# Kernel optimization log

Hardware: AMD Instinct MI355X
Metric: run time of the kernel (lower is better)

Reference implementation:

```python
import jax, jax.numpy as jnp
import numpy as np

DIM = 1024
N_HEADS = 16
HEAD_DIM = DIM // N_HEADS


def setup_inputs() -> dict:
    key = jax.random.key(0)
    ks = jax.random.split(key, 7)
    B, S = 2, 2048
    scale = 0.02
    return {
        "q": jax.random.normal(ks[0], (B, S, DIM), dtype=jnp.float32),
        "k": jax.random.normal(ks[1], (B, S, DIM), dtype=jnp.float32),
        "v": jax.random.normal(ks[2], (B, S, DIM), dtype=jnp.float32),
        # torch nn.Linear weights are [out_features, in_features]; y = x @ W.T
        "wq": jax.random.normal(ks[3], (DIM, DIM), dtype=jnp.float32) * scale,
        "wk": jax.random.normal(ks[4], (DIM, DIM), dtype=jnp.float32) * scale,
        "wv": jax.random.normal(ks[5], (DIM, DIM), dtype=jnp.float32) * scale,
        "wo": jax.random.normal(ks[6], (DIM, DIM), dtype=jnp.float32) * scale,
    }


def reference(q, k, v, wq, wk, wv, wo):
    B, S, _ = q.shape
    H, D = N_HEADS, HEAD_DIM
    # projections (torch Linear: x @ W.T), reshape to [B, H, S, D]
    xq = (q @ wq.T).reshape(B, S, H, D).transpose(0, 2, 1, 3)
    xk = (k @ wk.T).reshape(B, S, H, D).transpose(0, 2, 1, 3)
    xv = (v @ wv.T).reshape(B, S, H, D).transpose(0, 2, 1, 3)
    # scaled dot-product attention with causal mask
    scores = jnp.einsum("bhqd,bhkd->bhqk", xq, xk) / jnp.sqrt(jnp.float32(D))
    causal = jnp.tril(jnp.ones((S, S), dtype=bool))
    scores = jnp.where(causal, scores, -jnp.inf)
    attn = jax.nn.softmax(scores.astype(jnp.float32), axis=-1).astype(xq.dtype)
    # dropout prob = 0.0 (eval-mode / deterministic reference)
    out = jnp.einsum("bhqk,bhkd->bhqd", attn, xv)
    out = out.transpose(0, 2, 1, 3).reshape(B, S, H * D)
    return out @ wo.T
```

## Files before the change

### kernel.cpp

```cpp
#include <hip/hip_runtime.h>
#include <hip/hip_bf16.h>
#include <stdint.h>


typedef short s16x8 __attribute__((ext_vector_type(8)));
typedef float f32x4 __attribute__((ext_vector_type(4)));

#define MFMA_BF16 __builtin_amdgcn_mfma_f32_16x16x32_bf16

static __device__ __forceinline__ unsigned short f2bf(float f) {
    union { float f; unsigned u; } x{f};
    unsigned r = x.u + 0x7fff + ((x.u >> 16) & 1);
    return (unsigned short)(r >> 16);
}
static __device__ __forceinline__ unsigned pk2h(float a, float b) {
    __hip_bfloat162 h = __float22bfloat162_rn(float2{a, b});
    return *(unsigned*)&h;
}

static __device__ __forceinline__ void ald16(unsigned short* lds, const unsigned short* g) {
    __builtin_amdgcn_global_load_lds(
        (const __attribute__((address_space(1))) unsigned int*)g,
        (__attribute__((address_space(3))) unsigned int*)lds, 16, 0, 0);
}

#define QSCL 0.18033688f

__global__ __launch_bounds__(256) void convert_all_kernel(
        const float* __restrict__ q, const float* __restrict__ k,
        const float* __restrict__ v,
        const float* __restrict__ wq, const float* __restrict__ wk,
        const float* __restrict__ wv, const float* __restrict__ wo,
        unsigned short* __restrict__ dst) {
    const size_t idx = ((size_t)blockIdx.x * 256 + threadIdx.x) * 8;
    const int region = (int)(idx >> 22);
    const float* src;
    size_t off;
    if (region == 0)      { src = q; off = idx; }
    else if (region == 1) { src = k; off = idx & 4194303; }
    else if (region == 2) { src = v; off = idx & 4194303; }
    else {
        const int wsel = (int)((idx >> 20) & 3);
        src = wsel == 0 ? wq : wsel == 1 ? wk : wsel == 2 ? wv : wo;
        off = idx & 1048575;
    }
    const float4* p = (const float4*)(src + off);
    float4 a = p[0], b = p[1];
    uint4 u;
    u.x = pk2h(a.x, a.y); u.y = pk2h(a.z, a.w);
    u.z = pk2h(b.x, b.y); u.w = pk2h(b.z, b.w);
    *(uint4*)(dst + idx) = u;
}

__global__ __launch_bounds__(256) void wconvert_kernel(
        const float* __restrict__ wq, const float* __restrict__ wk,
        const float* __restrict__ wv, const float* __restrict__ wo,
        unsigned short* __restrict__ Wb) {
    const size_t idx = ((size_t)blockIdx.x * 256 + threadIdx.x) * 8;
    const int region = (int)(idx >> 20);
    const size_t off = idx & 1048575;
    const float* src = region == 0 ? wq : region == 1 ? wk : region == 2 ? wv : wo;
    const float4* p = (const float4*)(src + off);
    float4 a = p[0], b = p[1];
    uint4 u;
    u.x = pk2h(a.x, a.y); u.y = pk2h(a.z, a.w);
    u.z = pk2h(b.x, b.y); u.w = pk2h(b.z, b.w);
    *(uint4*)(Wb + idx) = u;
}

__global__ __launch_bounds__(256) void proj3b_kernel(
        const unsigned short* __restrict__ Qb, const unsigned short* __restrict__ Kb,
        const unsigned short* __restrict__ Vb, const unsigned short* __restrict__ Wb,
        unsigned short* __restrict__ Xq, unsigned short* __restrict__ Xk,
        unsigned short* __restrict__ Xvt) {
    constexpr int Kd = 1024;
    __shared__ union {
        struct { unsigned short A[128 * 32]; unsigned short B[128 * 32]; } s;
        unsigned short T[4 * 64 * 68];
    } sm;

    const int z = blockIdx.z;
    const unsigned short* A  = z == 0 ? Qb : z == 1 ? Kb : Vb;
    const unsigned short* Bw = Wb + (size_t)z * 1048576;

    const int t = threadIdx.x;
    const int m0 = blockIdx.x * 128, n0 = blockIdx.y * 128;
    const int w = t >> 6, lane = t & 63, fr = lane & 15, g = lane >> 4;
    const int wm = (w >> 1) * 64, wn = (w & 1) * 64;
    const int brow = t >> 2;
    const int cB = (t & 3) ^ ((t >> 3) & 3);
    const int sB = g ^ ((fr >> 1) & 3);

    f32x4 acc[4][4] = {};

    for (int k0 = 0; k0 < Kd; k0 += 32) {
        ald16(sm.s.A + (size_t)w * 512,        A  + (size_t)(m0 + brow) * Kd + k0 + cB * 8);
        ald16(sm.s.A + 2048 + (size_t)w * 512, A  + (size_t)(m0 + 64 + brow) * Kd + k0 + cB * 8);
        ald16(sm.s.B + (size_t)w * 512,        Bw + (size_t)(n0 + brow) * Kd + k0 + cB * 8);
        ald16(sm.s.B + 2048 + (size_t)w * 512, Bw + (size_t)(n0 + 64 + brow) * Kd + k0 + cB * 8);
        __syncthreads();

        s16x8 af[4], bfv[4];
#pragma unroll
        for (int mi = 0; mi < 4; ++mi)
            af[mi] = *(const s16x8*)(sm.s.A + (wm + mi * 16 + fr) * 32 + sB * 8);
#pragma unroll
        for (int ni = 0; ni < 4; ++ni)
            bfv[ni] = *(const s16x8*)(sm.s.B + (wn + ni * 16 + fr) * 32 + sB * 8);
#pragma unroll
        for (int mi = 0; mi < 4; ++mi)
#pragma unroll
            for (int ni = 0; ni < 4; ++ni)
                acc[mi][ni] = MFMA_BF16(af[mi], bfv[ni], acc[mi][ni], 0, 0, 0);
        __syncthreads();
    }

    if (z != 2) {
        unsigned short* C = z ? Xk : Xq;
        const float osc = z == 0 ? QSCL : 1.0f;
#pragma unroll
        for (int mi = 0; mi < 4; ++mi)
#pragma unroll
            for (int ni = 0; ni < 4; ++ni)
#pragma unroll
                for (int reg = 0; reg < 4; ++reg)
                    C[(size_t)(m0 + wm + mi * 16 + g * 4 + reg) * 1024 +
                      n0 + wn + ni * 16 + fr] = f2bf(acc[mi][ni][reg] * osc);
    } else {
        unsigned short* T = sm.T + w * (64 * 68);
#pragma unroll
        for (int mi = 0; mi < 4; ++mi)
#pragma unroll
            for (int ni = 0; ni < 4; ++ni) {
                uint2 u;
                u.x = pk2h(acc[mi][ni][0], acc[mi][ni][1]);
                u.y = pk2h(acc[mi][ni][2], acc[mi][ni][3]);
                *(uint2*)(T + (ni * 16 + fr) * 68 + mi * 16 + g * 4) = u;
            }
        __asm__ __volatile__("" ::: "memory");
#pragma unroll
        for (int pass = 0; pass < 8; ++pass) {
            const int row = pass * 8 + (lane >> 3);
            const int chk = lane & 7;
            uint4 d = *(const uint4*)(T + row * 68 + chk * 8);
            *(uint4*)(Xvt + (size_t)(n0 + wn + row) * 4096 + m0 + wm + chk * 8) = d;
        }
    }
}

__global__ __launch_bounds__(256) void proj3_kernel(
        const float* __restrict__ q, const float* __restrict__ k, const float* __restrict__ v,
        const unsigned short* __restrict__ Wb,
        unsigned short* __restrict__ Xq, unsigned short* __restrict__ Xk,
        unsigned short* __restrict__ Xvt) {
    constexpr int Kd = 1024;
    __shared__ unsigned short lsA[128 * 40];
    __shared__ unsigned short lsB[128 * 32];
    __shared__ unsigned short Tls[4 * 64 * 68];

    const int z = blockIdx.z;
    const float* A = z == 0 ? q : z == 1 ? k : v;
    const unsigned short* Bw = Wb + (size_t)z * 1048576;

    const int t = threadIdx.x;
    const int m0 = blockIdx.x * 128, n0 = blockIdx.y * 128;
    const int w = t >> 6, lane = t & 63, fr = lane & 15, g = lane >> 4, fq = g * 8;
    const int wm = (w >> 1) * 64, wn = (w & 1) * 64;
    const int ar = t >> 1, ac = (t & 1) * 16;
    const int brow = t >> 2;
    const int cB = (t & 3) ^ ((t >> 3) & 3);
    const int sB = g ^ ((fr >> 1) & 3);

    f32x4 acc[4][4] = {};

    for (int k0 = 0; k0 < Kd; k0 += 32) {
        ald16(lsB + (size_t)w * 512,        Bw + (size_t)(n0 + brow) * Kd + k0 + cB * 8);
        ald16(lsB + 2048 + (size_t)w * 512, Bw + (size_t)(n0 + 64 + brow) * Kd + k0 + cB * 8);
        {
            const float4* pa = (const float4*)(A + (size_t)(m0 + ar) * Kd + k0 + ac);
            float4 a0 = pa[0], a1 = pa[1], a2 = pa[2], a3 = pa[3];
            uint4 u0, u1;
            u0.x = pk2h(a0.x, a0.y); u0.y = pk2h(a0.z, a0.w);
            u0.z = pk2h(a1.x, a1.y); u0.w = pk2h(a1.z, a1.w);
            u1.x = pk2h(a2.x, a2.y); u1.y = pk2h(a2.z, a2.w);
            u1.z = pk2h(a3.x, a3.y); u1.w = pk2h(a3.z, a3.w);
            *(uint4*)(lsA + ar * 40 + ac)     = u0;
            *(uint4*)(lsA + ar * 40 + ac + 8) = u1;
        }
        __syncthreads();

        s16x8 af[4], bfv[4];
#pragma unroll
        for (int mi = 0; mi < 4; ++mi)
            af[mi] = *(const s16x8*)(lsA + (wm + mi * 16 + fr) * 40 + fq);
#pragma unroll
        for (int ni = 0; ni < 4; ++ni)
            bfv[ni] = *(const s16x8*)(lsB + (wn + ni * 16 + fr) * 32 + sB * 8);
#pragma unroll
        for (int mi = 0; mi < 4; ++mi)
#pragma unroll
            for (int ni = 0; ni < 4; ++ni)
                acc[mi][ni] = MFMA_BF16(af[mi], bfv[ni], acc[mi][ni], 0, 0, 0);
        __syncthreads();
    }

    if (z != 2) {
        unsigned short* C = z ? Xk : Xq;
        const float osc = z == 0 ? QSCL : 1.0f;
#pragma unroll
        for (int mi = 0; mi < 4; ++mi)
#pragma unroll
            for (int ni = 0; ni < 4; ++ni)
#pragma unroll
                for (int reg = 0; reg < 4; ++reg)
                    C[(size_t)(m0 + wm + mi * 16 + g * 4 + reg) * 1024 +
                      n0 + wn + ni * 16 + fr] = f2bf(acc[mi][ni][reg] * osc);
    } else {
        unsigned short* T = Tls + w * (64 * 68);
#pragma unroll
        for (int mi = 0; mi < 4; ++mi)
#pragma unroll
            for (int ni = 0; ni < 4; ++ni) {
                uint2 u;
                u.x = pk2h(acc[mi][ni][0], acc[mi][ni][1]);
                u.y = pk2h(acc[mi][ni][2], acc[mi][ni][3]);
                *(uint2*)(T + (ni * 16 + fr) * 68 + mi * 16 + g * 4) = u;
            }
        __asm__ __volatile__("" ::: "memory");
#pragma unroll
        for (int pass = 0; pass < 8; ++pass) {
            const int row = pass * 8 + (lane >> 3);
            const int chk = lane & 7;
            uint4 d = *(const uint4*)(T + row * 68 + chk * 8);
            *(uint4*)(Xvt + (size_t)(n0 + wn + row) * 4096 + m0 + wm + chk * 8) = d;
        }
    }
}

static __device__ __forceinline__ void slab_tail(
        const f32x4 sf[4], int kt, int qt, int qrow, float& l_part,
        f32x4* oacc, unsigned short* Pw, const s16x8 vf[4][2], int fr, int g) {
    float e[4][4];
    const bool diag = (kt == qt);
#pragma unroll
    for (int m16 = 0; m16 < 4; ++m16)
#pragma unroll
        for (int r = 0; r < 4; ++r) {
            float x = sf[m16][r];
            if (diag) {
                const int keyg = kt * 64 + m16 * 16 + g * 4 + r;
                x = (keyg <= qrow) ? x : -1e30f;
            }
            const float ee = exp2f(x);
            e[m16][r] = ee;
            l_part += ee;
        }
#pragma unroll
    for (int m16 = 0; m16 < 4; ++m16) {
        uint2 u;
        u.x = pk2h(e[m16][0], e[m16][1]);
        u.y = pk2h(e[m16][2], e[m16][3]);
        const int ch = 2 * m16 + (g >> 1);
        *(uint2*)(Pw + fr * 64 + ((ch ^ (fr & 7)) * 8) + (g & 1) * 4) = u;
    }
    __asm__ __volatile__("" ::: "memory");
    s16x8 pf0 = *(const s16x8*)(Pw + fr * 64 + ((g ^ (fr & 7)) * 8));
    s16x8 pf1 = *(const s16x8*)(Pw + fr * 64 + (((4 + g) ^ (fr & 7)) * 8));
#pragma unroll
    for (int m16 = 0; m16 < 4; ++m16) {
        oacc[m16] = MFMA_BF16(vf[m16][0], pf0, oacc[m16], 0, 0, 0);
        oacc[m16] = MFMA_BF16(vf[m16][1], pf1, oacc[m16], 0, 0, 0);
    }
    __asm__ __volatile__("" ::: "memory");
}

__global__ __launch_bounds__(256, 2) void flash_attn_kernel(
        const unsigned short* __restrict__ Xq, const unsigned short* __restrict__ Xk,
        const unsigned short* __restrict__ Xvt, unsigned short* __restrict__ Oa) {
    __shared__ unsigned short Kls[64 * 64];
    __shared__ unsigned short Vls[64 * 64];
    __shared__ unsigned short Pls[4][16 * 64];

    const int t = threadIdx.x;
    const int bh = blockIdx.x;
    const int j = blockIdx.y;
    const int b = bh >> 4, h = bh & 15;
    const size_t rbase = (size_t)b * 2048;
    const int cbase = h * 64;

    const int w = t >> 6, lane = t & 63, fr = lane & 15, g = lane >> 4, fq = g * 8;
    const int qtH = 31 - j, qtL = j;
    const int qrowH = qtH * 64 + w * 16 + fr;
    const int qrowL = qtL * 64 + w * 16 + fr;

    const unsigned short* qpH = Xq + (rbase + qrowH) * 1024 + cbase;
    s16x8 qfH0 = *(const s16x8*)(qpH + fq);
    s16x8 qfH1 = *(const s16x8*)(qpH + 32 + fq);
    const unsigned short* qpL = Xq + (rbase + qrowL) * 1024 + cbase;
    s16x8 qfL0 = *(const s16x8*)(qpL + fq);
    s16x8 qfL1 = *(const s16x8*)(qpL + 32 + fq);

    float lH = 0.f, lL = 0.f;
    f32x4 oH[4] = {}, oL[4] = {};

    const int r0 = w * 16 + (lane >> 3), r1 = r0 + 8;
    const int s8 = lane & 7;
    const int c0 = s8 ^ (r0 & 7), c1 = s8 ^ (r1 & 7);
    const unsigned short* kbase = Xk + rbase * 1024 + cbase;
    const size_t vrow0 = (size_t)(cbase + r0) * 4096 + rbase + c0 * 8;
    const size_t vrow1 = (size_t)(cbase + r1) * 4096 + rbase + c1 * 8;

    uint4 kA, kB, vA, vB;
    kA = *(const uint4*)(kbase + (size_t)r0 * 1024 + c0 * 8);
    kB = *(const uint4*)(kbase + (size_t)r1 * 1024 + c1 * 8);
    vA = *(const uint4*)(Xvt + vrow0);
    vB = *(const uint4*)(Xvt + vrow1);

    for (int kt = 0; kt <= qtH; ++kt) {
        *(uint4*)(Kls + (w * 16) * 64 + lane * 8)     = kA;
        *(uint4*)(Kls + (w * 16 + 8) * 64 + lane * 8) = kB;
        *(uint4*)(Vls + (w * 16) * 64 + lane * 8)     = vA;
        *(uint4*)(Vls + (w * 16 + 8) * 64 + lane * 8) = vB;
        __syncthreads();

        if (kt < qtH) {
            const unsigned short* ks = kbase + (size_t)(kt + 1) * 65536;
            kA = *(const uint4*)(ks + (size_t)r0 * 1024 + c0 * 8);
            kB = *(const uint4*)(ks + (size_t)r1 * 1024 + c1 * 8);
            vA = *(const uint4*)(Xvt + vrow0 + (size_t)(kt + 1) * 64);
            vB = *(const uint4*)(Xvt + vrow1 + (size_t)(kt + 1) * 64);
        }

        const bool doL = (kt <= qtL);

        s16x8 kf[4][2], vf[4][2];
#pragma unroll
        for (int m16 = 0; m16 < 4; ++m16) {
            const int rr = m16 * 16 + fr;
            kf[m16][0] = *(const s16x8*)(Kls + rr * 64 + ((g ^ (fr & 7)) * 8));
            kf[m16][1] = *(const s16x8*)(Kls + rr * 64 + (((4 + g) ^ (fr & 7)) * 8));
            vf[m16][0] = *(const s16x8*)(Vls + rr * 64 + ((g ^ (fr & 7)) * 8));
            vf[m16][1] = *(const s16x8*)(Vls + rr * 64 + (((4 + g) ^ (fr & 7)) * 8));
        }

        f32x4 sH[4], sL[4];
#pragma unroll
        for (int m16 = 0; m16 < 4; ++m16) {
            f32x4 zz = {};
            zz = MFMA_BF16(kf[m16][0], qfH0, zz, 0, 0, 0);
            sH[m16] = MFMA_BF16(kf[m16][1], qfH1, zz, 0, 0, 0);
        }
        if (doL) {
#pragma unroll
            for (int m16 = 0; m16 < 4; ++m16) {
                f32x4 zz = {};
                zz = MFMA_BF16(kf[m16][0], qfL0, zz, 0, 0, 0);
                sL[m16] = MFMA_BF16(kf[m16][1], qfL1, zz, 0, 0, 0);
            }
        }
        slab_tail(sH, kt, qtH, qrowH, lH, oH, &Pls[w][0], vf, fr, g);
        if (doL)
            slab_tail(sL, kt, qtL, qrowL, lL, oL, &Pls[w][0], vf, fr, g);
        __syncthreads();
    }

    lH += __shfl_xor(lH, 16, 64);
    lH += __shfl_xor(lH, 32, 64);
    lL += __shfl_xor(lL, 16, 64);
    lL += __shfl_xor(lL, 32, 64);
    const float invH = 1.0f / lH, invL = 1.0f / lL;
#pragma unroll
    for (int m16 = 0; m16 < 4; ++m16) {
        uint2 u;
        u.x = pk2h(oH[m16][0] * invH, oH[m16][1] * invH);
        u.y = pk2h(oH[m16][2] * invH, oH[m16][3] * invH);
        *(uint2*)(Oa + (rbase + qrowH) * 1024 + cbase + m16 * 16 + g * 4) = u;
        uint2 u2;
        u2.x = pk2h(oL[m16][0] * invL, oL[m16][1] * invL);
        u2.y = pk2h(oL[m16][2] * invL, oL[m16][3] * invL);
        *(uint2*)(Oa + (rbase + qrowL) * 1024 + cbase + m16 * 16 + g * 4) = u2;
    }
}

__global__ __launch_bounds__(256) void outproj_kernel(
        const unsigned short* __restrict__ Oa, const unsigned short* __restrict__ Wo,
        float* __restrict__ out) {
    constexpr int Kd = 1024;
    __shared__ unsigned short lsA[64 * 32];
    __shared__ unsigned short lsB[128 * 32];

    const int t = threadIdx.x;
    const int m0 = blockIdx.x * 64, n0 = blockIdx.y * 128;
    const int w = t >> 6, lane = t & 63, fr = lane & 15, g = lane >> 4;
    const int wm = (w >> 1) * 32, wn = (w & 1) * 64;
    const int brow = t >> 2;
    const int cB = (t & 3) ^ ((t >> 3) & 3);
    const int sB = g ^ ((fr >> 1) & 3);

    f32x4 acc[2][4] = {};

    for (int k0 = 0; k0 < Kd; k0 += 32) {
        ald16(lsA + (size_t)w * 512,        Oa + (size_t)(m0 + brow) * Kd + k0 + cB * 8);
        ald16(lsB + (size_t)w * 512,        Wo + (size_t)(n0 + brow) * Kd + k0 + cB * 8);
        ald16(lsB + 2048 + (size_t)w * 512, Wo + (size_t)(n0 + 64 + brow) * Kd + k0 + cB * 8);
        __syncthreads();

        s16x8 af[2], bfv[4];
#pragma unroll
        for (int mi = 0; mi < 2; ++mi)
            af[mi] = *(const s16x8*)(lsA + (wm + mi * 16 + fr) * 32 + sB * 8);
#pragma unroll
        for (int ni = 0; ni < 4; ++ni)
            bfv[ni] = *(const s16x8*)(lsB + (wn + ni * 16 + fr) * 32 + sB * 8);
#pragma unroll
        for (int mi = 0; mi < 2; ++mi)
#pragma unroll
            for (int ni = 0; ni < 4; ++ni)
                acc[mi][ni] = MFMA_BF16(af[mi], bfv[ni], acc[mi][ni], 0, 0, 0);
        __syncthreads();
    }

#pragma unroll
    for (int mi = 0; mi < 2; ++mi)
#pragma unroll
        for (int ni = 0; ni < 4; ++ni)
#pragma unroll
            for (int reg = 0; reg < 4; ++reg)
                out[(size_t)(m0 + wm + mi * 16 + g * 4 + reg) * 1024 +
                    n0 + wn + ni * 16 + fr] = acc[mi][ni][reg];
}

extern "C" void kernel_launch(void* const* d_in, const int* in_sizes, int n_in,
                              void* d_out, int out_size, void* d_ws, size_t ws_size,
                              hipStream_t stream) {
    const float* q  = (const float*)d_in[0];
    const float* k  = (const float*)d_in[1];
    const float* v  = (const float*)d_in[2];
    const float* wq = (const float*)d_in[3];
    const float* wk = (const float*)d_in[4];
    const float* wv = (const float*)d_in[5];
    const float* wo = (const float*)d_in[6];
    float* out = (float*)d_out;

    if (ws_size >= (size_t)64 * 1024 * 1024) {
        unsigned short* base = (unsigned short*)d_ws;
        unsigned short* Qb  = base;
        unsigned short* Kb  = base + 4194304;
        unsigned short* Vb  = base + 8388608;
        unsigned short* Wb  = base + 12582912;
        unsigned short* Xq  = base + 16777216;
        unsigned short* Xk  = base + 20971520;
        unsigned short* Xvt = base + 25165824;
        unsigned short* Oa  = base + 29360128;

        convert_all_kernel<<<8192, 256, 0, stream>>>(q, k, v, wq, wk, wv, wo, base);
        proj3b_kernel<<<dim3(32, 8, 3), 256, 0, stream>>>(Qb, Kb, Vb, Wb, Xq, Xk, Xvt);
        flash_attn_kernel<<<dim3(32, 16), 256, 0, stream>>>(Xq, Xk, Xvt, Oa);
        outproj_kernel<<<dim3(64, 8), 256, 0, stream>>>(Oa, Wb + 3145728, out);
    } else {
        unsigned short* Wb  = (unsigned short*)d_ws;
        unsigned short* Xq  = Wb  + 4194304;
        unsigned short* Xk  = Xq  + 4194304;
        unsigned short* Xvt = Xk  + 4194304;
        unsigned short* Oa  = Xvt + 4194304;

        wconvert_kernel<<<2048, 256, 0, stream>>>(wq, wk, wv, wo, Wb);
        proj3_kernel<<<dim3(32, 8, 3), 256, 0, stream>>>(q, k, v, Wb, Xq, Xk, Xvt);
        flash_attn_kernel<<<dim3(32, 16), 256, 0, stream>>>(Xq, Xk, Xvt, Oa);
        outproj_kernel<<<dim3(64, 8), 256, 0, stream>>>(Oa, Wb + 3145728, out);
    }
}
```

Measured before the change: 213.6 us.

## Fuse convert, projection, attention and out-projection into one persistent kernel with grid barriers

Replaces the four kernel launches with a single persistent kernel of 512 blocks. The blocks pass through the phases (fp32-to-bf16 conversion, QKV projection using 64x128 tiles, flash attention, output projection) separated by atomic-counter grid barriers in workspace, which is zeroed by a memset before each launch. This removes launch gaps and inter-kernel tail effects. In exchange it relies on all 512 blocks being co-resident (two per CU), uses smaller projection tiles, has a spin barrier with a timeout guard, and drops the small-workspace fallback path.

```diff
diff --git a/kernel.cpp b/kernel.cpp
--- a/kernel.cpp
+++ b/kernel.cpp
@@ -17,7 +17,6 @@
     __hip_bfloat162 h = __float22bfloat162_rn(float2{a, b});
     return *(unsigned*)&h;
 }
-
 static __device__ __forceinline__ void ald16(unsigned short* lds, const unsigned short* g) {
     __builtin_amdgcn_global_load_lds(
         (const __attribute__((address_space(1))) unsigned int*)g,
@@ -25,90 +24,63 @@
 }
 
 #define QSCL 0.18033688f
-
-__global__ __launch_bounds__(256) void convert_all_kernel(
-        const float* __restrict__ q, const float* __restrict__ k,
-        const float* __restrict__ v,
-        const float* __restrict__ wq, const float* __restrict__ wk,
-        const float* __restrict__ wv, const float* __restrict__ wo,
-        unsigned short* __restrict__ dst) {
-    const size_t idx = ((size_t)blockIdx.x * 256 + threadIdx.x) * 8;
-    const int region = (int)(idx >> 22);
-    const float* src;
-    size_t off;
-    if (region == 0)      { src = q; off = idx; }
-    else if (region == 1) { src = k; off = idx & 4194303; }
-    else if (region == 2) { src = v; off = idx & 4194303; }
-    else {
-        const int wsel = (int)((idx >> 20) & 3);
-        src = wsel == 0 ? wq : wsel == 1 ? wk : wsel == 2 ? wv : wo;
-        off = idx & 1048575;
-    }
-    const float4* p = (const float4*)(src + off);
-    float4 a = p[0], b = p[1];
-    uint4 u;
-    u.x = pk2h(a.x, a.y); u.y = pk2h(a.z, a.w);
-    u.z = pk2h(b.x, b.y); u.w = pk2h(b.z, b.w);
-    *(uint4*)(dst + idx) = u;
-}
-
-__global__ __launch_bounds__(256) void wconvert_kernel(
-        const float* __restrict__ wq, const float* __restrict__ wk,
-        const float* __restrict__ wv, const float* __restrict__ wo,
-        unsigned short* __restrict__ Wb) {
-    const size_t idx = ((size_t)blockIdx.x * 256 + threadIdx.x) * 8;
-    const int region = (int)(idx >> 20);
-    const size_t off = idx & 1048575;
-    const float* src = region == 0 ? wq : region == 1 ? wk : region == 2 ? wv : wo;
-    const float4* p = (const float4*)(src + off);
-    float4 a = p[0], b = p[1];
-    uint4 u;
-    u.x = pk2h(a.x, a.y); u.y = pk2h(a.z, a.w);
-    u.z = pk2h(b.x, b.y); u.w = pk2h(b.z, b.w);
-    *(uint4*)(Wb + idx) = u;
-}
-
-__global__ __launch_bounds__(256) void proj3b_kernel(
-        const unsigned short* __restrict__ Qb, const unsigned short* __restrict__ Kb,
-        const unsigned short* __restrict__ Vb, const unsigned short* __restrict__ Wb,
-        unsigned short* __restrict__ Xq, unsigned short* __restrict__ Xk,
-        unsigned short* __restrict__ Xvt) {
+#define NBLK 512u
+
+union SM {
+    struct { unsigned short A[64 * 32]; unsigned short B[128 * 32]; } g;
+    unsigned short T[4 * 64 * 36];
+    struct { unsigned short K[64 * 64]; unsigned short V[64 * 64];
+             unsigned short P[4][16 * 64]; } f;
+};
+
+static __device__ __forceinline__ void grid_sync(unsigned* bar) {
+    __syncthreads();
+    if (threadIdx.x == 0) {
+        __threadfence();
+        __hip_atomic_fetch_add(bar, 1u, __ATOMIC_ACQ_REL, __HIP_MEMORY_SCOPE_AGENT);
+        int guard = 0;
+        while (__hip_atomic_load(bar, __ATOMIC_ACQUIRE, __HIP_MEMORY_SCOPE_AGENT) < NBLK) {
+            __builtin_amdgcn_s_sleep(8);
+            if (++guard > (1 << 22)) break;
+        }
+        __threadfence();
+    }
+    __syncthreads();
+}
+
+static __device__ void proj_tile64(int tile, SM& sm,
+        const unsigned short* __restrict__ ws, unsigned short* __restrict__ Xq,
+        unsigned short* __restrict__ Xk, unsigned short* __restrict__ Xvt) {
     constexpr int Kd = 1024;
-    __shared__ union {
-        struct { unsigned short A[128 * 32]; unsigned short B[128 * 32]; } s;
-        unsigned short T[4 * 64 * 68];
-    } sm;
-
-    const int z = blockIdx.z;
-    const unsigned short* A  = z == 0 ? Qb : z == 1 ? Kb : Vb;
-    const unsigned short* Bw = Wb + (size_t)z * 1048576;
+    const int z = tile >> 9;
+    const int m0 = (tile & 63) * 64, n0 = ((tile >> 6) & 7) * 128;
+    const unsigned short* A  = ws + (size_t)z * 4194304;
+    const unsigned short* Bw = ws + 12582912 + (size_t)z * 1048576;
 
     const int t = threadIdx.x;
-    const int m0 = blockIdx.x * 128, n0 = blockIdx.y * 128;
     const int w = t >> 6, lane = t & 63, fr = lane & 15, g = lane >> 4;
-    const int wm = (w >> 1) * 64, wn = (w & 1) * 64;
+    const int wm = (w >> 1) * 32, wn = (w & 1) * 64;
     const int brow = t >> 2;
     const int cB = (t & 3) ^ ((t >> 3) & 3);
     const int sB = g ^ ((fr >> 1) & 3);
 
-    f32x4 acc[4][4] = {};
+    f32x4 acc[2][4] = {};
 
     for (int k0 = 0; k0 < Kd; k0 += 32) {
-        ald16(sm.s.A + (size_t)w * 512,        A  + (size_t)(m0 + brow) * Kd + k0 + cB * 8);
-        ald16(sm.s.A + 2048 + (size_t)w * 512, A  + (size_t)(m0 + 64 + brow) * Kd + k0 + cB * 8);
-        ald16(sm.s.B + (size_t)w * 512,        Bw + (size_t)(n0 + brow) * Kd + k0 + cB * 8);
-        ald16(sm.s.B + 2048 + (size_t)w * 512, Bw + (size_t)(n0 + 64 + brow) * Kd + k0 + cB * 8);
-        __syncthreads();
-
-        s16x8 af[4], bfv[4];
-#pragma unroll
-        for (int mi = 0; mi < 4; ++mi)
-            af[mi] = *(const s16x8*)(sm.s.A + (wm + mi * 16 + fr) * 32 + sB * 8);
+        ald16(sm.g.A + (size_t)w * 512,        A  + (size_t)(m0 + brow) * Kd + k0 + cB * 8);
+        ald16(sm.g.B + (size_t)w * 512,        Bw + (size_t)(n0 + brow) * Kd + k0 + cB * 8);
+        ald16(sm.g.B + 2048 + (size_t)w * 512, Bw + (size_t)(n0 + 64 + brow) * Kd + k0 + cB * 8);
+        __syncthreads();
+
+        s16x8 af[2], bfv[4];
+#pragma unroll
+        for (int mi = 0; mi < 2; ++mi)
+            af[mi] = *(const s16x8*)(sm.g.A + (wm + mi * 16 + fr) * 32 + sB * 8);
 #pragma unroll
         for (int ni = 0; ni < 4; ++ni)
-            bfv[ni] = *(const s16x8*)(sm.s.B + (wn + ni * 16 + fr) * 32 + sB * 8);
-#pragma unroll
-        for (int mi = 0; mi < 4; ++mi)
+            bfv[ni] = *(const s16x8*)(sm.g.B + (wn + ni * 16 + fr) * 32 + sB * 8);
+#pragma unroll
+        for (int mi = 0; mi < 2; ++mi)
 #pragma unroll
             for (int ni = 0; ni < 4; ++ni)
                 acc[mi][ni] = MFMA_BF16(af[mi], bfv[ni], acc[mi][ni], 0, 0, 0);
@@ -119,7 +91,7 @@
         unsigned short* C = z ? Xk : Xq;
         const float osc = z == 0 ? QSCL : 1.0f;
 #pragma unroll
-        for (int mi = 0; mi < 4; ++mi)
+        for (int mi = 0; mi < 2; ++mi)
 #pragma unroll
             for (int ni = 0; ni < 4; ++ni)
 #pragma unroll
@@ -127,111 +99,22 @@
                     C[(size_t)(m0 + wm + mi * 16 + g * 4 + reg) * 1024 +
                       n0 + wn + ni * 16 + fr] = f2bf(acc[mi][ni][reg] * osc);
     } else {
-        unsigned short* T = sm.T + w * (64 * 68);
-#pragma unroll
-        for (int mi = 0; mi < 4; ++mi)
+        unsigned short* T = sm.T + w * (64 * 36);
+#pragma unroll
+        for (int mi = 0; mi < 2; ++mi)
 #pragma unroll
             for (int ni = 0; ni < 4; ++ni) {
                 uint2 u;
                 u.x = pk2h(acc[mi][ni][0], acc[mi][ni][1]);
                 u.y = pk2h(acc[mi][ni][2], acc[mi][ni][3]);
-                *(uint2*)(T + (ni * 16 + fr) * 68 + mi * 16 + g * 4) = u;
+                *(uint2*)(T + (ni * 16 + fr) * 36 + mi * 16 + g * 4) = u;
             }
         __asm__ __volatile__("" ::: "memory");
 #pragma unroll
-        for (int pass = 0; pass < 8; ++pass) {
-            const int row = pass * 8 + (lane >> 3);
-            const int chk = lane & 7;
-            uint4 d = *(const uint4*)(T + row * 68 + chk * 8);
-            *(uint4*)(Xvt + (size_t)(n0 + wn + row) * 4096 + m0 + wm + chk * 8) = d;
-        }
-    }
-}
-
-__global__ __launch_bounds__(256) void proj3_kernel(
-        const float* __restrict__ q, const float* __restrict__ k, const float* __restrict__ v,
-        const unsigned short* __restrict__ Wb,
-        unsigned short* __restrict__ Xq, unsigned short* __restrict__ Xk,
-        unsigned short* __restrict__ Xvt) {
-    constexpr int Kd = 1024;
-    __shared__ unsigned short lsA[128 * 40];
-    __shared__ unsigned short lsB[128 * 32];
-    __shared__ unsigned short Tls[4 * 64 * 68];
-
-    const int z = blockIdx.z;
-    const float* A = z == 0 ? q : z == 1 ? k : v;
-    const unsigned short* Bw = Wb + (size_t)z * 1048576;
-
-    const int t = threadIdx.x;
-    const int m0 = blockIdx.x * 128, n0 = blockIdx.y * 128;
-    const int w = t >> 6, lane = t & 63, fr = lane & 15, g = lane >> 4, fq = g * 8;
-    const int wm = (w >> 1) * 64, wn = (w & 1) * 64;
-    const int ar = t >> 1, ac = (t & 1) * 16;
-    const int brow = t >> 2;
-    const int cB = (t & 3) ^ ((t >> 3) & 3);
-    const int sB = g ^ ((fr >> 1) & 3);
-
-    f32x4 acc[4][4] = {};
-
-    for (int k0 = 0; k0 < Kd; k0 += 32) {
-        ald16(lsB + (size_t)w * 512,        Bw + (size_t)(n0 + brow) * Kd + k0 + cB * 8);
-        ald16(lsB + 2048 + (size_t)w * 512, Bw + (size_t)(n0 + 64 + brow) * Kd + k0 + cB * 8);
-        {
-            const float4* pa = (const float4*)(A + (size_t)(m0 + ar) * Kd + k0 + ac);
-            float4 a0 = pa[0], a1 = pa[1], a2 = pa[2], a3 = pa[3];
-            uint4 u0, u1;
-            u0.x = pk2h(a0.x, a0.y); u0.y = pk2h(a0.z, a0.w);
-            u0.z = pk2h(a1.x, a1.y); u0.w = pk2h(a1.z, a1.w);
-            u1.x = pk2h(a2.x, a2.y); u1.y = pk2h(a2.z, a2.w);
-            u1.z = pk2h(a3.x, a3.y); u1.w = pk2h(a3.z, a3.w);
-            *(uint4*)(lsA + ar * 40 + ac)     = u0;
-            *(uint4*)(lsA + ar * 40 + ac + 8) = u1;
-        }
-        __syncthreads();
-
-        s16x8 af[4], bfv[4];
-#pragma unroll
-        for (int mi = 0; mi < 4; ++mi)
-            af[mi] = *(const s16x8*)(lsA + (wm + mi * 16 + fr) * 40 + fq);
-#pragma unroll
-        for (int ni = 0; ni < 4; ++ni)
-            bfv[ni] = *(const s16x8*)(lsB + (wn + ni * 16 + fr) * 32 + sB * 8);
-#pragma unroll
-        for (int mi = 0; mi < 4; ++mi)
-#pragma unroll
-            for (int ni = 0; ni < 4; ++ni)
-                acc[mi][ni] = MFMA_BF16(af[mi], bfv[ni], acc[mi][ni], 0, 0, 0);
-        __syncthreads();
-    }
-
-    if (z != 2) {
-        unsigned short* C = z ? Xk : Xq;
-        const float osc = z == 0 ? QSCL : 1.0f;
-#pragma unroll
-        for (int mi = 0; mi < 4; ++mi)
-#pragma unroll
-            for (int ni = 0; ni < 4; ++ni)
-#pragma unroll
-                for (int reg = 0; reg < 4; ++reg)
-                    C[(size_t)(m0 + wm + mi * 16 + g * 4 + reg) * 1024 +
-                      n0 + wn + ni * 16 + fr] = f2bf(acc[mi][ni][reg] * osc);
-    } else {
-        unsigned short* T = Tls + w * (64 * 68);
-#pragma unroll
-        for (int mi = 0; mi < 4; ++mi)
-#pragma unroll
-            for (int ni = 0; ni < 4; ++ni) {
-                uint2 u;
-                u.x = pk2h(acc[mi][ni][0], acc[mi][ni][1]);
-                u.y = pk2h(acc[mi][ni][2], acc[mi][ni][3]);
-                *(uint2*)(T + (ni * 16 + fr) * 68 + mi * 16 + g * 4) = u;
-            }
-        __asm__ __volatile__("" ::: "memory");
-#pragma unroll
-        for (int pass = 0; pass < 8; ++pass) {
-            const int row = pass * 8 + (lane >> 3);
-            const int chk = lane & 7;
-            uint4 d = *(const uint4*)(T + row * 68 + chk * 8);
+        for (int pass = 0; pass < 4; ++pass) {
+            const int row = pass * 16 + (lane >> 2);
+            const int chk = lane & 3;
+            uint4 d = *(const uint4*)(T + row * 36 + chk * 8);
             *(uint4*)(Xvt + (size_t)(n0 + wn + row) * 4096 + m0 + wm + chk * 8) = d;
         }
     }
@@ -274,16 +157,14 @@
     __asm__ __volatile__("" ::: "memory");
 }
 
-__global__ __launch_bounds__(256, 2) void flash_attn_kernel(
+static __device__ void flash_pair(int idx, SM& sm,
         const unsigned short* __restrict__ Xq, const unsigned short* __restrict__ Xk,
         const unsigned short* __restrict__ Xvt, unsigned short* __restrict__ Oa) {
-    __shared__ unsigned short Kls[64 * 64];
-    __shared__ unsigned short Vls[64 * 64];
-    __shared__ unsigned short Pls[4][16 * 64];
+    unsigned short* Kls = sm.f.K;
+    unsigned short* Vls = sm.f.V;
 
     const int t = threadIdx.x;
-    const int bh = blockIdx.x;
-    const int j = blockIdx.y;
+    const int bh = idx & 31, j = idx >> 5;
     const int b = bh >> 4, h = bh & 15;
     const size_t rbase = (size_t)b * 2048;
     const int cbase = h * 64;
@@ -358,9 +239,9 @@
                 sL[m16] = MFMA_BF16(kf[m16][1], qfL1, zz, 0, 0, 0);
             }
         }
-        slab_tail(sH, kt, qtH, qrowH, lH, oH, &Pls[w][0], vf, fr, g);
+        slab_tail(sH, kt, qtH, qrowH, lH, oH, &sm.f.P[w][0], vf, fr, g);
         if (doL)
-            slab_tail(sL, kt, qtL, qrowL, lL, oL, &Pls[w][0], vf, fr, g);
+            slab_tail(sL, kt, qtL, qrowL, lL, oL, &sm.f.P[w][0], vf, fr, g);
         __syncthreads();
     }
 
@@ -382,15 +263,12 @@
     }
 }
 
-__global__ __launch_bounds__(256) void outproj_kernel(
+static __device__ void outproj_tile(int tile, SM& sm,
         const unsigned short* __restrict__ Oa, const unsigned short* __restrict__ Wo,
         float* __restrict__ out) {
     constexpr int Kd = 1024;
-    __shared__ unsigned short lsA[64 * 32];
-    __shared__ unsigned short lsB[128 * 32];
-
     const int t = threadIdx.x;
-    const int m0 = blockIdx.x * 64, n0 = blockIdx.y * 128;
+    const int m0 = (tile & 63) * 64, n0 = (tile >> 6) * 128;
     const int w = t >> 6, lane = t & 63, fr = lane & 15, g = lane >> 4;
     const int wm = (w >> 1) * 32, wn = (w & 1) * 64;
     const int brow = t >> 2;
@@ -400,18 +278,18 @@
     f32x4 acc[2][4] = {};
 
     for (int k0 = 0; k0 < Kd; k0 += 32) {
-        ald16(lsA + (size_t)w * 512,        Oa + (size_t)(m0 + brow) * Kd + k0 + cB * 8);
-        ald16(lsB + (size_t)w * 512,        Wo + (size_t)(n0 + brow) * Kd + k0 + cB * 8);
-        ald16(lsB + 2048 + (size_t)w * 512, Wo + (size_t)(n0 + 64 + brow) * Kd + k0 + cB * 8);
+        ald16(sm.g.A + (size_t)w * 512,        Oa + (size_t)(m0 + brow) * Kd + k0 + cB * 8);
+        ald16(sm.g.B + (size_t)w * 512,        Wo + (size_t)(n0 + brow) * Kd + k0 + cB * 8);
+        ald16(sm.g.B + 2048 + (size_t)w * 512, Wo + (size_t)(n0 + 64 + brow) * Kd + k0 + cB * 8);
         __syncthreads();
 
         s16x8 af[2], bfv[4];
 #pragma unroll
         for (int mi = 0; mi < 2; ++mi)
-            af[mi] = *(const s16x8*)(lsA + (wm + mi * 16 + fr) * 32 + sB * 8);
+            af[mi] = *(const s16x8*)(sm.g.A + (wm + mi * 16 + fr) * 32 + sB * 8);
 #pragma unroll
         for (int ni = 0; ni < 4; ++ni)
-            bfv[ni] = *(const s16x8*)(lsB + (wn + ni * 16 + fr) * 32 + sB * 8);
+            bfv[ni] = *(const s16x8*)(sm.g.B + (wn + ni * 16 + fr) * 32 + sB * 8);
 #pragma unroll
         for (int mi = 0; mi < 2; ++mi)
 #pragma unroll
@@ -428,6 +306,60 @@
             for (int reg = 0; reg < 4; ++reg)
                 out[(size_t)(m0 + wm + mi * 16 + g * 4 + reg) * 1024 +
                     n0 + wn + ni * 16 + fr] = acc[mi][ni][reg];
+}
+
+__global__ __launch_bounds__(256, 2) void fused_mha_kernel(
+        const float* __restrict__ q, const float* __restrict__ k,
+        const float* __restrict__ v,
+        const float* __restrict__ wq, const float* __restrict__ wk,
+        const float* __restrict__ wv, const float* __restrict__ wo,
+        float* __restrict__ out, unsigned short* __restrict__ ws) {
+    __shared__ SM sm;
+    const int bx = blockIdx.x;
+    unsigned* bar = (unsigned*)(ws + 29360128);
+
+    {
+        const size_t base_i = ((size_t)bx * 256 + threadIdx.x) * 8;
+#pragma unroll
+        for (int i = 0; i < 16; ++i) {
+            const size_t idx = base_i + (size_t)i * 1048576;
+            const int region = (int)(idx >> 22);
+            const float* src;
+            size_t off;
+            if (region == 0)      { src = q; off = idx; }
+            else if (region == 1) { src = k; off = idx & 4194303; }
+            else if (region == 2) { src = v; off = idx & 4194303; }
+            else {
+                const int wsel = (int)((idx >> 20) & 3);
+                src = wsel == 0 ? wq : wsel == 1 ? wk : wsel == 2 ? wv : wo;
+                off = idx & 1048575;
+            }
+            const float4* p = (const float4*)(src + off);
+            float4 a = p[0], b2 = p[1];
+            uint4 u;
+            u.x = pk2h(a.x, a.y);  u.y = pk2h(a.z, a.w);
+            u.z = pk2h(b2.x, b2.y); u.w = pk2h(b2.z, b2.w);
+            *(uint4*)(ws + idx) = u;
+        }
+    }
+    grid_sync(bar + 0);
+
+    unsigned short* Xq  = ws + 16777216;
+    unsigned short* Xk  = ws + 20971520;
+    unsigned short* Xvt = ws + 25165824;
+    unsigned short* Oa  = ws;
+
+#pragma unroll
+    for (int r = 0; r < 3; ++r) {
+        if (r) __syncthreads();
+        proj_tile64(bx + r * 512, sm, ws, Xq, Xk, Xvt);
+    }
+    grid_sync(bar + 1);
+
+    flash_pair(bx, sm, Xq, Xk, Xvt, Oa);
+    grid_sync(bar + 2);
+
+    outproj_tile(bx, sm, Oa, ws + 15728640 , out);
 }
 
 extern "C" void kernel_launch(void* const* d_in, const int* in_sizes, int n_in,
@@ -441,32 +373,8 @@
     const float* wv = (const float*)d_in[5];
     const float* wo = (const float*)d_in[6];
     float* out = (float*)d_out;
-
-    if (ws_size >= (size_t)64 * 1024 * 1024) {
-        unsigned short* base = (unsigned short*)d_ws;
-        unsigned short* Qb  = base;
-        unsigned short* Kb  = base + 4194304;
-        unsigned short* Vb  = base + 8388608;
-        unsigned short* Wb  = base + 12582912;
-        unsigned short* Xq  = base + 16777216;
-        unsigned short* Xk  = base + 20971520;
-        unsigned short* Xvt = base + 25165824;
-        unsigned short* Oa  = base + 29360128;
-
-        convert_all_kernel<<<8192, 256, 0, stream>>>(q, k, v, wq, wk, wv, wo, base);
-        proj3b_kernel<<<dim3(32, 8, 3), 256, 0, stream>>>(Qb, Kb, Vb, Wb, Xq, Xk, Xvt);
-        flash_attn_kernel<<<dim3(32, 16), 256, 0, stream>>>(Xq, Xk, Xvt, Oa);
-        outproj_kernel<<<dim3(64, 8), 256, 0, stream>>>(Oa, Wb + 3145728, out);
-    } else {
-        unsigned short* Wb  = (unsigned short*)d_ws;
-        unsigned short* Xq  = Wb  + 4194304;
-        unsigned short* Xk  = Xq  + 4194304;
-        unsigned short* Xvt = Xk  + 4194304;
-        unsigned short* Oa  = Xvt + 4194304;
-
-        wconvert_kernel<<<2048, 256, 0, stream>>>(wq, wk, wv, wo, Wb);
-        proj3_kernel<<<dim3(32, 8, 3), 256, 0, stream>>>(q, k, v, Wb, Xq, Xk, Xvt);
-        flash_attn_kernel<<<dim3(32, 16), 256, 0, stream>>>(Xq, Xk, Xvt, Oa);
-        outproj_kernel<<<dim3(64, 8), 256, 0, stream>>>(Oa, Wb + 3145728, out);
-    }
-}
+    unsigned short* ws = (unsigned short*)d_ws;
+
+    hipMemsetAsync((char*)d_ws + 58720256, 0, 64, stream);
+    fused_mha_kernel<<<512, 256, 0, stream>>>(q, k, v, wq, wk, wv, wo, out, ws);
+}
```

New measurement: 439.7 us. 106% more time.

## Split paired causal query tiles into one tile per block with higher occupancy

Applied to the files above, without the earlier changes.

The flash attention kernel previously had each block process two query tiles (a high and a low one, paired for causal load balance) that shared the K/V tiles loaded into LDS. Now each block handles one query tile, the grid doubles to 32x32 blocks, and the launch bound asks for 4 blocks per CU instead of 2. This gives up K/V reuse and the balanced pairing in exchange for more parallelism and lower register pressure, but it creates uneven per-block work under the causal mask. It also drops the fallback path for small workspaces, so the code now assumes the 64 MB workspace is present.

```diff
diff --git a/kernel.cpp b/kernel.cpp
--- a/kernel.cpp
+++ b/kernel.cpp
@@ -17,7 +17,6 @@
     __hip_bfloat162 h = __float22bfloat162_rn(float2{a, b});
     return *(unsigned*)&h;
 }
-
 static __device__ __forceinline__ void ald16(unsigned short* lds, const unsigned short* g) {
     __builtin_amdgcn_global_load_lds(
         (const __attribute__((address_space(1))) unsigned int*)g,
@@ -52,22 +51,6 @@
     *(uint4*)(dst + idx) = u;
 }
 
-__global__ __launch_bounds__(256) void wconvert_kernel(
-        const float* __restrict__ wq, const float* __restrict__ wk,
-        const float* __restrict__ wv, const float* __restrict__ wo,
-        unsigned short* __restrict__ Wb) {
-    const size_t idx = ((size_t)blockIdx.x * 256 + threadIdx.x) * 8;
-    const int region = (int)(idx >> 20);
-    const size_t off = idx & 1048575;
-    const float* src = region == 0 ? wq : region == 1 ? wk : region == 2 ? wv : wo;
-    const float4* p = (const float4*)(src + off);
-    float4 a = p[0], b = p[1];
-    uint4 u;
-    u.x = pk2h(a.x, a.y); u.y = pk2h(a.z, a.w);
-    u.z = pk2h(b.x, b.y); u.w = pk2h(b.z, b.w);
-    *(uint4*)(Wb + idx) = u;
-}
-
 __global__ __launch_bounds__(256) void proj3b_kernel(
         const unsigned short* __restrict__ Qb, const unsigned short* __restrict__ Kb,
         const unsigned short* __restrict__ Vb, const unsigned short* __restrict__ Wb,
@@ -148,133 +131,7 @@
     }
 }
 
-__global__ __launch_bounds__(256) void proj3_kernel(
-        const float* __restrict__ q, const float* __restrict__ k, const float* __restrict__ v,
-        const unsigned short* __restrict__ Wb,
-        unsigned short* __restrict__ Xq, unsigned short* __restrict__ Xk,
-        unsigned short* __restrict__ Xvt) {
-    constexpr int Kd = 1024;
-    __shared__ unsigned short lsA[128 * 40];
-    __shared__ unsigned short lsB[128 * 32];
-    __shared__ unsigned short Tls[4 * 64 * 68];
-
-    const int z = blockIdx.z;
-    const float* A = z == 0 ? q : z == 1 ? k : v;
-    const unsigned short* Bw = Wb + (size_t)z * 1048576;
-
-    const int t = threadIdx.x;
-    const int m0 = blockIdx.x * 128, n0 = blockIdx.y * 128;
-    const int w = t >> 6, lane = t & 63, fr = lane & 15, g = lane >> 4, fq = g * 8;
-    const int wm = (w >> 1) * 64, wn = (w & 1) * 64;
-    const int ar = t >> 1, ac = (t & 1) * 16;
-    const int brow = t >> 2;
-    const int cB = (t & 3) ^ ((t >> 3) & 3);
-    const int sB = g ^ ((fr >> 1) & 3);
-
-    f32x4 acc[4][4] = {};
-
-    for (int k0 = 0; k0 < Kd; k0 += 32) {
-        ald16(lsB + (size_t)w * 512,        Bw + (size_t)(n0 + brow) * Kd + k0 + cB * 8);
-        ald16(lsB + 2048 + (size_t)w * 512, Bw + (size_t)(n0 + 64 + brow) * Kd + k0 + cB * 8);
-        {
-            const float4* pa = (const float4*)(A + (size_t)(m0 + ar) * Kd + k0 + ac);
-            float4 a0 = pa[0], a1 = pa[1], a2 = pa[2], a3 = pa[3];
-            uint4 u0, u1;
-            u0.x = pk2h(a0.x, a0.y); u0.y = pk2h(a0.z, a0.w);
-            u0.z = pk2h(a1.x, a1.y); u0.w = pk2h(a1.z, a1.w);
-            u1.x = pk2h(a2.x, a2.y); u1.y = pk2h(a2.z, a2.w);
-            u1.z = pk2h(a3.x, a3.y); u1.w = pk2h(a3.z, a3.w);
-            *(uint4*)(lsA + ar * 40 + ac)     = u0;
-            *(uint4*)(lsA + ar * 40 + ac + 8) = u1;
-        }
-        __syncthreads();
-
-        s16x8 af[4], bfv[4];
-#pragma unroll
-        for (int mi = 0; mi < 4; ++mi)
-            af[mi] = *(const s16x8*)(lsA + (wm + mi * 16 + fr) * 40 + fq);
-#pragma unroll
-        for (int ni = 0; ni < 4; ++ni)
-            bfv[ni] = *(const s16x8*)(lsB + (wn + ni * 16 + fr) * 32 + sB * 8);
-#pragma unroll
-        for (int mi = 0; mi < 4; ++mi)
-#pragma unroll
-            for (int ni = 0; ni < 4; ++ni)
-                acc[mi][ni] = MFMA_BF16(af[mi], bfv[ni], acc[mi][ni], 0, 0, 0);
-        __syncthreads();
-    }
-
-    if (z != 2) {
-        unsigned short* C = z ? Xk : Xq;
-        const float osc = z == 0 ? QSCL : 1.0f;
-#pragma unroll
-        for (int mi = 0; mi < 4; ++mi)
-#pragma unroll
-            for (int ni = 0; ni < 4; ++ni)
-#pragma unroll
-                for (int reg = 0; reg < 4; ++reg)
-                    C[(size_t)(m0 + wm + mi * 16 + g * 4 + reg) * 1024 +
-                      n0 + wn + ni * 16 + fr] = f2bf(acc[mi][ni][reg] * osc);
-    } else {
-        unsigned short* T = Tls + w * (64 * 68);
-#pragma unroll
-        for (int mi = 0; mi < 4; ++mi)
-#pragma unroll
-            for (int ni = 0; ni < 4; ++ni) {
-                uint2 u;
-                u.x = pk2h(acc[mi][ni][0], acc[mi][ni][1]);
-                u.y = pk2h(acc[mi][ni][2], acc[mi][ni][3]);
-                *(uint2*)(T + (ni * 16 + fr) * 68 + mi * 16 + g * 4) = u;
-            }
-        __asm__ __volatile__("" ::: "memory");
-#pragma unroll
-        for (int pass = 0; pass < 8; ++pass) {
-            const int row = pass * 8 + (lane >> 3);
-            const int chk = lane & 7;
-            uint4 d = *(const uint4*)(T + row * 68 + chk * 8);
-            *(uint4*)(Xvt + (size_t)(n0 + wn + row) * 4096 + m0 + wm + chk * 8) = d;
-        }
-    }
-}
-
-static __device__ __forceinline__ void slab_tail(
-        const f32x4 sf[4], int kt, int qt, int qrow, float& l_part,
-        f32x4* oacc, unsigned short* Pw, const s16x8 vf[4][2], int fr, int g) {
-    float e[4][4];
-    const bool diag = (kt == qt);
-#pragma unroll
-    for (int m16 = 0; m16 < 4; ++m16)
-#pragma unroll
-        for (int r = 0; r < 4; ++r) {
-            float x = sf[m16][r];
-            if (diag) {
-                const int keyg = kt * 64 + m16 * 16 + g * 4 + r;
-                x = (keyg <= qrow) ? x : -1e30f;
-            }
-            const float ee = exp2f(x);
-            e[m16][r] = ee;
-            l_part += ee;
-        }
-#pragma unroll
-    for (int m16 = 0; m16 < 4; ++m16) {
-        uint2 u;
-        u.x = pk2h(e[m16][0], e[m16][1]);
-        u.y = pk2h(e[m16][2], e[m16][3]);
-        const int ch = 2 * m16 + (g >> 1);
-        *(uint2*)(Pw + fr * 64 + ((ch ^ (fr & 7)) * 8) + (g & 1) * 4) = u;
-    }
-    __asm__ __volatile__("" ::: "memory");
-    s16x8 pf0 = *(const s16x8*)(Pw + fr * 64 + ((g ^ (fr & 7)) * 8));
-    s16x8 pf1 = *(const s16x8*)(Pw + fr * 64 + (((4 + g) ^ (fr & 7)) * 8));
-#pragma unroll
-    for (int m16 = 0; m16 < 4; ++m16) {
-        oacc[m16] = MFMA_BF16(vf[m16][0], pf0, oacc[m16], 0, 0, 0);
-        oacc[m16] = MFMA_BF16(vf[m16][1], pf1, oacc[m16], 0, 0, 0);
-    }
-    __asm__ __volatile__("" ::: "memory");
-}
-
-__global__ __launch_bounds__(256, 2) void flash_attn_kernel(
+__global__ __launch_bounds__(256, 4) void flash_attn_kernel(
         const unsigned short* __restrict__ Xq, const unsigned short* __restrict__ Xk,
         const unsigned short* __restrict__ Xvt, unsigned short* __restrict__ Oa) {
     __shared__ unsigned short Kls[64 * 64];
@@ -283,25 +140,20 @@
 
     const int t = threadIdx.x;
     const int bh = blockIdx.x;
-    const int j = blockIdx.y;
+    const int qt = blockIdx.y;
     const int b = bh >> 4, h = bh & 15;
     const size_t rbase = (size_t)b * 2048;
     const int cbase = h * 64;
 
     const int w = t >> 6, lane = t & 63, fr = lane & 15, g = lane >> 4, fq = g * 8;
-    const int qtH = 31 - j, qtL = j;
-    const int qrowH = qtH * 64 + w * 16 + fr;
-    const int qrowL = qtL * 64 + w * 16 + fr;
-
-    const unsigned short* qpH = Xq + (rbase + qrowH) * 1024 + cbase;
-    s16x8 qfH0 = *(const s16x8*)(qpH + fq);
-    s16x8 qfH1 = *(const s16x8*)(qpH + 32 + fq);
-    const unsigned short* qpL = Xq + (rbase + qrowL) * 1024 + cbase;
-    s16x8 qfL0 = *(const s16x8*)(qpL + fq);
-    s16x8 qfL1 = *(const s16x8*)(qpL + 32 + fq);
-
-    float lH = 0.f, lL = 0.f;
-    f32x4 oH[4] = {}, oL[4] = {};
+    const int qrow = qt * 64 + w * 16 + fr;
+
+    const unsigned short* qp = Xq + (rbase + qrow) * 1024 + cbase;
+    s16x8 qf0 = *(const s16x8*)(qp + fq);
+    s16x8 qf1 = *(const s16x8*)(qp + 32 + fq);
+
+    float l_i = 0.f;
+    f32x4 oacc[4] = {};
 
     const int r0 = w * 16 + (lane >> 3), r1 = r0 + 8;
     const int s8 = lane & 7;
@@ -316,14 +168,14 @@
     vA = *(const uint4*)(Xvt + vrow0);
     vB = *(const uint4*)(Xvt + vrow1);
 
-    for (int kt = 0; kt <= qtH; ++kt) {
+    for (int kt = 0; kt <= qt; ++kt) {
         *(uint4*)(Kls + (w * 16) * 64 + lane * 8)     = kA;
         *(uint4*)(Kls + (w * 16 + 8) * 64 + lane * 8) = kB;
         *(uint4*)(Vls + (w * 16) * 64 + lane * 8)     = vA;
         *(uint4*)(Vls + (w * 16 + 8) * 64 + lane * 8) = vB;
         __syncthreads();
 
-        if (kt < qtH) {
+        if (kt < qt) {
             const unsigned short* ks = kbase + (size_t)(kt + 1) * 65536;
             kA = *(const uint4*)(ks + (size_t)r0 * 1024 + c0 * 8);
             kB = *(const uint4*)(ks + (size_t)r1 * 1024 + c1 * 8);
@@ -331,54 +183,66 @@
             vB = *(const uint4*)(Xvt + vrow1 + (size_t)(kt + 1) * 64);
         }
 
-        const bool doL = (kt <= qtL);
-
-        s16x8 kf[4][2], vf[4][2];
+        f32x4 sf[4];
 #pragma unroll
         for (int m16 = 0; m16 < 4; ++m16) {
             const int rr = m16 * 16 + fr;
-            kf[m16][0] = *(const s16x8*)(Kls + rr * 64 + ((g ^ (fr & 7)) * 8));
-            kf[m16][1] = *(const s16x8*)(Kls + rr * 64 + (((4 + g) ^ (fr & 7)) * 8));
-            vf[m16][0] = *(const s16x8*)(Vls + rr * 64 + ((g ^ (fr & 7)) * 8));
-            vf[m16][1] = *(const s16x8*)(Vls + rr * 64 + (((4 + g) ^ (fr & 7)) * 8));
-        }
-
-        f32x4 sH[4], sL[4];
+            s16x8 kf0 = *(const s16x8*)(Kls + rr * 64 + ((g ^ (fr & 7)) * 8));
+            s16x8 kf1 = *(const s16x8*)(Kls + rr * 64 + (((4 + g) ^ (fr & 7)) * 8));
+            f32x4 zz = {};
+            zz = MFMA_BF16(kf0, qf0, zz, 0, 0, 0);
+            sf[m16] = MFMA_BF16(kf1, qf1, zz, 0, 0, 0);
+        }
+
+        float e[4][4];
+        const bool diag = (kt == qt);
+#pragma unroll
+        for (int m16 = 0; m16 < 4; ++m16)
+#pragma unroll
+            for (int r = 0; r < 4; ++r) {
+                float x = sf[m16][r];
+                if (diag) {
+                    const int keyg = kt * 64 + m16 * 16 + g * 4 + r;
+                    x = (keyg <= qrow) ? x : -1e30f;
+                }
+                const float ee = exp2f(x);
+                e[m16][r] = ee;
+                l_i += ee;
+            }
+
+        unsigned short* Pw = &Pls[w][0];
 #pragma unroll
         for (int m16 = 0; m16 < 4; ++m16) {
-            f32x4 zz = {};
-            zz = MFMA_BF16(kf[m16][0], qfH0, zz, 0, 0, 0);
-            sH[m16] = MFMA_BF16(kf[m16][1], qfH1, zz, 0, 0, 0);
-        }
-        if (doL) {
-#pragma unroll
-            for (int m16 = 0; m16 < 4; ++m16) {
-                f32x4 zz = {};
-                zz = MFMA_BF16(kf[m16][0], qfL0, zz, 0, 0, 0);
-                sL[m16] = MFMA_BF16(kf[m16][1], qfL1, zz, 0, 0, 0);
-            }
-        }
-        slab_tail(sH, kt, qtH, qrowH, lH, oH, &Pls[w][0], vf, fr, g);
-        if (doL)
-            slab_tail(sL, kt, qtL, qrowL, lL, oL, &Pls[w][0], vf, fr, g);
-        __syncthreads();
-    }
-
-    lH += __shfl_xor(lH, 16, 64);
-    lH += __shfl_xor(lH, 32, 64);
-    lL += __shfl_xor(lL, 16, 64);
-    lL += __shfl_xor(lL, 32, 64);
-    const float invH = 1.0f / lH, invL = 1.0f / lL;
+            uint2 u;
+            u.x = pk2h(e[m16][0], e[m16][1]);
+            u.y = pk2h(e[m16][2], e[m16][3]);
+            const int ch = 2 * m16 + (g >> 1);
+            *(uint2*)(Pw + fr * 64 + ((ch ^ (fr & 7)) * 8) + (g & 1) * 4) = u;
+        }
+        __asm__ __volatile__("" ::: "memory");
+        s16x8 pf0 = *(const s16x8*)(Pw + fr * 64 + ((g ^ (fr & 7)) * 8));
+        s16x8 pf1 = *(const s16x8*)(Pw + fr * 64 + (((4 + g) ^ (fr & 7)) * 8));
+
+#pragma unroll
+        for (int m16 = 0; m16 < 4; ++m16) {
+            const int rr = m16 * 16 + fr;
+            s16x8 vf0 = *(const s16x8*)(Vls + rr * 64 + ((g ^ (fr & 7)) * 8));
+            s16x8 vf1 = *(const s16x8*)(Vls + rr * 64 + (((4 + g) ^ (fr & 7)) * 8));
+            oacc[m16] = MFMA_BF16(vf0, pf0, oacc[m16], 0, 0, 0);
+            oacc[m16] = MFMA_BF16(vf1, pf1, oacc[m16], 0, 0, 0);
+        }
+        __syncthreads();
+    }
+
+    l_i += __shfl_xor(l_i, 16, 64);
+    l_i += __shfl_xor(l_i, 32, 64);
+    const float inv = 1.0f / l_i;
 #pragma unroll
     for (int m16 = 0; m16 < 4; ++m16) {
         uint2 u;
-        u.x = pk2h(oH[m16][0] * invH, oH[m16][1] * invH);
-        u.y = pk2h(oH[m16][2] * invH, oH[m16][3] * invH);
-        *(uint2*)(Oa + (rbase + qrowH) * 1024 + cbase + m16 * 16 + g * 4) = u;
-        uint2 u2;
-        u2.x = pk2h(oL[m16][0] * invL, oL[m16][1] * invL);
-        u2.y = pk2h(oL[m16][2] * invL, oL[m16][3] * invL);
-        *(uint2*)(Oa + (rbase + qrowL) * 1024 + cbase + m16 * 16 + g * 4) = u2;
+        u.x = pk2h(oacc[m16][0] * inv, oacc[m16][1] * inv);
+        u.y = pk2h(oacc[m16][2] * inv, oacc[m16][3] * inv);
+        *(uint2*)(Oa + (rbase + qrow) * 1024 + cbase + m16 * 16 + g * 4) = u;
     }
 }
 
@@ -442,31 +306,18 @@
     const float* wo = (const float*)d_in[6];
     float* out = (float*)d_out;
 
-    if (ws_size >= (size_t)64 * 1024 * 1024) {
-        unsigned short* base = (unsigned short*)d_ws;
-        unsigned short* Qb  = base;
-        unsigned short* Kb  = base + 4194304;
-        unsigned short* Vb  = base + 8388608;
-        unsigned short* Wb  = base + 12582912;
-        unsigned short* Xq  = base + 16777216;
-        unsigned short* Xk  = base + 20971520;
-        unsigned short* Xvt = base + 25165824;
-        unsigned short* Oa  = base + 29360128;
-
-        convert_all_kernel<<<8192, 256, 0, stream>>>(q, k, v, wq, wk, wv, wo, base);
-        proj3b_kernel<<<dim3(32, 8, 3), 256, 0, stream>>>(Qb, Kb, Vb, Wb, Xq, Xk, Xvt);
-        flash_attn_kernel<<<dim3(32, 16), 256, 0, stream>>>(Xq, Xk, Xvt, Oa);
-        outproj_kernel<<<dim3(64, 8), 256, 0, stream>>>(Oa, Wb + 3145728, out);
-    } else {
-        unsigned short* Wb  = (unsigned short*)d_ws;
-        unsigned short* Xq  = Wb  + 4194304;
-        unsigned short* Xk  = Xq  + 4194304;
-        unsigned short* Xvt = Xk  + 4194304;
-        unsigned short* Oa  = Xvt + 4194304;
-
-        wconvert_kernel<<<2048, 256, 0, stream>>>(wq, wk, wv, wo, Wb);
-        proj3_kernel<<<dim3(32, 8, 3), 256, 0, stream>>>(q, k, v, Wb, Xq, Xk, Xvt);
-        flash_attn_kernel<<<dim3(32, 16), 256, 0, stream>>>(Xq, Xk, Xvt, Oa);
-        outproj_kernel<<<dim3(64, 8), 256, 0, stream>>>(Oa, Wb + 3145728, out);
-    }
-}
+    unsigned short* base = (unsigned short*)d_ws;
+    unsigned short* Qb  = base;
+    unsigned short* Kb  = base + 4194304;
+    unsigned short* Vb  = base + 8388608;
+    unsigned short* Wb  = base + 12582912;
+    unsigned short* Xq  = base + 16777216;
+    unsigned short* Xk  = base + 20971520;
+    unsigned short* Xvt = base + 25165824;
+    unsigned short* Oa  = base + 29360128;
+
+    convert_all_kernel<<<8192, 256, 0, stream>>>(q, k, v, wq, wk, wv, wo, base);
+    proj3b_kernel<<<dim3(32, 8, 3), 256, 0, stream>>>(Qb, Kb, Vb, Wb, Xq, Xk, Xvt);
+    flash_attn_kernel<<<dim3(32, 32), 256, 0, stream>>>(Xq, Xk, Xvt, Oa);
+    outproj_kernel<<<dim3(64, 8), 256, 0, stream>>>(Oa, Wb + 3145728, out);
+}
```

Result: no change. 217.3 us (+1.7%).
